# Kernel tuning notes

Measured on AMD Instinct MI355X. Metric: run time of the kernel, lower is better.

Reference implementation:

```python
import jax, jax.numpy as jnp
import numpy as np

NUM_EMBEDDINGS = 1024
EMBEDDING_DIM = 64
COMMITMENT_COST = 0.25


def setup_inputs() -> dict:
    key = jax.random.key(0)
    k1, k2 = jax.random.split(key)
    inputs = jax.random.normal(k1, (64, 2048, EMBEDDING_DIM), dtype=jnp.float32)
    # nn.Embedding weight init: uniform(-1/K, 1/K)
    lim = 1.0 / NUM_EMBEDDINGS
    weight = jax.random.uniform(k2, (NUM_EMBEDDINGS, EMBEDDING_DIM),
                                dtype=jnp.float32, minval=-lim, maxval=lim)
    return {"inputs": inputs, "weight": weight}


def reference(inputs, weight):
    # inputs: [B, T, D], weight: [K, D]
    flat = inputs.reshape(-1, EMBEDDING_DIM)              # [N, D]
    distances = (jnp.sum(flat * flat, axis=1, keepdims=True)
                 + jnp.sum(weight * weight, axis=1)
                 - 2.0 * flat @ weight.T)
    encoding_indices = jnp.argmin(distances, axis=1)[:, None]  # [N, 1]
    quantized = weight[encoding_indices[:, 0]].reshape(inputs.shape)
    # detached quantized vs inputs (commitment), quantized vs detached inputs (codebook)
    e_latent_loss = jnp.mean((jax.lax.stop_gradient(quantized) - inputs) ** 2)
    q_latent_loss = jnp.mean((quantized - jax.lax.stop_gradient(inputs)) ** 2)
    loss = q_latent_loss + COMMITMENT_COST * e_latent_loss
    # straight-through estimator
    quantized_st = inputs + jax.lax.stop_gradient(quantized - inputs)
    return (loss, quantized_st, encoding_indices)
```

## Files before the change

kernel.cpp:

```cpp
#include <hip/hip_runtime.h>

#define NROWS   131072
#define DIM     64
#define K       1024
#define QOFF    1
#define IDXOFF  8388609
#define NSCR    1024
#define NFIN    512

typedef float    f32x4 __attribute__((ext_vector_type(4)));
typedef _Float16 f16x8 __attribute__((ext_vector_type(8)));

__device__ __forceinline__ float np_norm64(const float* v) {
    #pragma clang fp contract(off)
    float r[8];
    #pragma unroll
    for (int k = 0; k < 8; ++k) r[k] = v[k] * v[k];
    #pragma unroll
    for (int i = 8; i < 64; i += 8)
        #pragma unroll
        for (int k = 0; k < 8; ++k) r[k] += v[i + k] * v[i + k];
    return ((r[0] + r[1]) + (r[2] + r[3])) + ((r[4] + r[5]) + (r[6] + r[7]));
}
__device__ __forceinline__ float exact_dot64(const float* xr, const float* __restrict__ e) {
    float a0 = 0.f, a1 = 0.f, a2 = 0.f, a3 = 0.f;
    #pragma unroll
    for (int i = 0; i < 64; i += 4) {
        a0 = fmaf(xr[i + 0], e[i + 0], a0);
        a1 = fmaf(xr[i + 1], e[i + 1], a1);
        a2 = fmaf(xr[i + 2], e[i + 2], a2);
        a3 = fmaf(xr[i + 3], e[i + 3], a3);
    }
    return (a0 + a1) + (a2 + a3);
}
__device__ __forceinline__ float exact_d(float cr, float sej, float dot) {
    #pragma clang fp contract(off)
    float t = cr + sej;
    return t - 2.0f * dot;
}

__global__ void vq_prep(const float* __restrict__ w, unsigned short* __restrict__ Gf,
                        float* __restrict__ wT, float* __restrict__ se,
                        float* __restrict__ se20, int* __restrict__ gcnt) {
    int gid = blockIdx.x * 256 + threadIdx.x;
    if (gid < 2) gcnt[gid] = 0;
    int lane = gid & 63, c = (gid >> 6) & 1, ntile = gid >> 7;
    int code = ntile * 16 + (lane & 15);
    int k0 = c * 32 + (lane >> 4) * 8;
    const float* rowp = w + code * 64 + k0;
    f16x8 h8;
    #pragma unroll
    for (int j = 0; j < 8; ++j) h8[j] = (_Float16)(rowp[j] * 1024.0f);
    *(f16x8*)(Gf + gid * 8) = h8;
    #pragma unroll
    for (int t = 0; t < 8; ++t) {
        int flat = t * 8192 + gid;
        int i = flat >> 10, j = flat & 1023;
        wT[flat] = w[j * 64 + i];
    }
    if (gid < K) {
        #pragma clang fp contract(off)
        const float* e = w + gid * 64;
        float r[8];
        #pragma unroll
        for (int k2 = 0; k2 < 8; ++k2) r[k2] = e[k2] * e[k2];
        #pragma unroll
        for (int i = 8; i < 64; i += 8)
            #pragma unroll
            for (int k2 = 0; k2 < 8; ++k2) r[k2] += e[i + k2] * e[i + k2];
        float v = ((r[0] + r[1]) + (r[2] + r[3])) + ((r[4] + r[5]) + (r[6] + r[7]));
        se[gid] = v;
        se20[gid] = v * 1048576.0f;
    }
}

__global__ __launch_bounds__(256, 4) void vq_screen(
    const float* __restrict__ x, const float* __restrict__ w,
    const unsigned short* __restrict__ Gf, const float* __restrict__ se20,
    float* __restrict__ out, float* __restrict__ partial, int* __restrict__ gcnt,
    int* __restrict__ pairRows, int* __restrict__ pairJJ, int* __restrict__ fullRows) {
    __shared__ float sSe[1024];
    __shared__ float sPart[4];
    __shared__ int sCnt[2], sBase[2];
    __shared__ int sPairRow[128], sPairJJ[128], sFullRow[128];
    const int tid  = threadIdx.x;
    const int wave = tid >> 6, lane = tid & 63;
    const int quad = lane >> 4, m16 = lane & 15;
    const int wrow0 = blockIdx.x * 128 + wave * 32;

    if (tid < 2) sCnt[tid] = 0;
    #pragma unroll
    for (int t = 0; t < 4; ++t) sSe[t * 256 + tid] = se20[t * 256 + tid];

    f16x8 Ah[2][2];
    float Sloc[2] = {0.f, 0.f};
    #pragma unroll
    for (int mt = 0; mt < 2; ++mt)
        #pragma unroll
        for (int c = 0; c < 2; ++c) {
            const float* p = x + (wrow0 + mt * 16 + m16) * 64 + c * 32 + quad * 8;
            f32x4 u0 = *(const f32x4*)p;
            f32x4 u1 = *(const f32x4*)(p + 4);
            #pragma unroll
            for (int j = 0; j < 8; ++j) {
                float xv = (j < 4) ? u0[j] : u1[j - 4];
                Ah[mt][c][j] = (_Float16)xv;
                Sloc[mt] += fabsf(xv);
            }
        }
    #pragma unroll
    for (int mt = 0; mt < 2; ++mt) {
        Sloc[mt] += __shfl_xor(Sloc[mt], 16, 64);
        Sloc[mt] += __shfl_xor(Sloc[mt], 32, 64);
    }

    int m1[2][4], m2[2][4], m3[2][4];
    #pragma unroll
    for (int mt = 0; mt < 2; ++mt)
        #pragma unroll
        for (int r = 0; r < 4; ++r) {
            m1[mt][r] = 0x7fffffff; m2[mt][r] = 0x7fffffff; m3[mt][r] = 0x7fffffff;
        }

    __syncthreads();

    #pragma unroll 8
    for (int t = 0; t < 64; ++t) {
        f16x8 B0 = *(const f16x8*)(Gf + t * 1024 + lane * 8);
        f16x8 B1 = *(const f16x8*)(Gf + t * 1024 + 512 + lane * 8);
        float sen = sSe[t * 16 + m16];
        int jn = t * 16 + m16;
        #pragma unroll
        for (int mt = 0; mt < 2; ++mt) {
            f32x4 acc = {0.f, 0.f, 0.f, 0.f};
            acc = __builtin_amdgcn_mfma_f32_16x16x32_f16(Ah[mt][0], B0, acc, 0, 0, 0);
            acc = __builtin_amdgcn_mfma_f32_16x16x32_f16(Ah[mt][1], B1, acc, 0, 0, 0);
            #pragma unroll
            for (int r = 0; r < 4; ++r) {
                float kf = fmaf(acc[r], -2048.0f, sen);
                int q = (int)kf;
                int key = (int)((unsigned)q << 10) | jn;
                int a  = max(m2[mt][r], key);
                int t2 = max(m1[mt][r], key);
                m3[mt][r] = min(m3[mt][r], a);
                m2[mt][r] = min(m2[mt][r], t2);
                m1[mt][r] = min(m1[mt][r], key);
            }
        }
    }

    #pragma unroll
    for (int mask = 1; mask <= 8; mask <<= 1) {
        #pragma unroll
        for (int mt = 0; mt < 2; ++mt)
            #pragma unroll
            for (int r = 0; r < 4; ++r) {
                int b1 = __shfl_xor(m1[mt][r], mask, 64);
                int b2 = __shfl_xor(m2[mt][r], mask, 64);
                int b3 = __shfl_xor(m3[mt][r], mask, 64);
                int lo1 = min(m1[mt][r], b1), hi1 = max(m1[mt][r], b1);
                int lo2 = min(m2[mt][r], b2);
                m1[mt][r] = lo1;
                m2[mt][r] = min(hi1, lo2);
                m3[mt][r] = min(max(hi1, lo2), min(m3[mt][r], b3));
            }
    }

    int jd[2][4];
    #pragma unroll
    for (int mt = 0; mt < 2; ++mt)
        #pragma unroll
        for (int r = 0; r < 4; ++r) {
            int k1 = m1[mt][r], k2 = m2[mt][r], k3 = m3[mt][r];
            int g21 = (k2 >> 10) - (k1 >> 10);
            int g31 = (k3 >> 10) - (k1 >> 10);
            int j1 = k1 & 1023;
            float Srow = __shfl(Sloc[mt], quad * 4 + r, 64);
            int mq = (int)(Srow * 2.002f) + 5;
            jd[mt][r] = (g21 > mq) ? j1 : -1;
            if (m16 == 0) {
                int rowG = wrow0 + mt * 16 + quad * 4 + r;
                if (g21 > mq) {
                    out[IDXOFF + rowG] = (float)j1;
                } else if (g31 > mq) {
                    int p = atomicAdd(&sCnt[0], 1);
                    sPairRow[p] = rowG; sPairJJ[p] = j1 | ((k2 & 1023) << 10);
                } else {
                    int p = atomicAdd(&sCnt[1], 1);
                    sFullRow[p] = rowG;
                }
            }
        }

    float part = 0.f;
    #pragma unroll
    for (int i = 0; i < 32; ++i) {
        int jr = __shfl(jd[i >> 4][i & 3], ((i & 15) >> 2) * 16, 64);
        if (jr >= 0) {
            #pragma clang fp contract(off)
            int rowG = wrow0 + i;
            float xv = x[rowG * 64 + lane];
            float wv = w[jr * 64 + lane];
            float diff = wv - xv;
            part += diff * diff;
            out[QOFF + rowG * 64 + lane] = xv + diff;
        }
    }
    for (int off = 32; off > 0; off >>= 1) part += __shfl_down(part, off, 64);
    if (lane == 0) sPart[wave] = part;
    __syncthreads();
    if (tid == 0) {
        partial[blockIdx.x] = (sPart[0] + sPart[1]) + (sPart[2] + sPart[3]);
        int np_ = sCnt[0], nf = sCnt[1];
        sBase[0] = np_ ? atomicAdd(&gcnt[0], np_) : 0;
        sBase[1] = nf  ? atomicAdd(&gcnt[1], nf)  : 0;
    }
    __syncthreads();
    if (tid < sCnt[0]) {
        int d = sBase[0] + tid;
        pairRows[d] = sPairRow[tid]; pairJJ[d] = sPairJJ[tid];
    }
    if (tid < sCnt[1]) fullRows[sBase[1] + tid] = sFullRow[tid];
}

__global__ __launch_bounds__(256) void vq_finish(
    const float* __restrict__ x, const float* __restrict__ w, const float* __restrict__ wT,
    const float* __restrict__ se, float* __restrict__ out, float* __restrict__ partial,
    const int* __restrict__ gcnt, const int* __restrict__ pairRows,
    const int* __restrict__ pairJJ, const int* __restrict__ fullRows) {
    __shared__ float sPart[4];
    const int tid = threadIdx.x;
    const int lane = tid & 63, wave = tid >> 6;
    const int nPair = gcnt[0], nFull = gcnt[1];
    const int gthread = blockIdx.x * 256 + tid, nThreads = gridDim.x * 256;
    const int gwave = blockIdx.x * 4 + wave,   nWaves = gridDim.x * 4;
    float part = 0.f;

    for (int i = gthread; i < nPair; i += nThreads) {
        int row = pairRows[i], jj = pairJJ[i];
        int ja = jj & 1023, jb = (jj >> 10) & 1023;
        if (ja > jb) { int t = ja; ja = jb; jb = t; }
        float xr[64];
        const f32x4* xp = (const f32x4*)(x + row * 64);
        #pragma unroll
        for (int t = 0; t < 16; ++t) {
            f32x4 v = xp[t];
            xr[4 * t] = v[0]; xr[4 * t + 1] = v[1]; xr[4 * t + 2] = v[2]; xr[4 * t + 3] = v[3];
        }
        float cr = np_norm64(xr);
        float da = exact_d(cr, se[ja], exact_dot64(xr, w + ja * 64));
        float db = exact_d(cr, se[jb], exact_dot64(xr, w + jb * 64));
        int win = (db < da) ? jb : ja;
        out[IDXOFF + row] = (float)win;
        const float* e = w + win * 64;
        {
            #pragma clang fp contract(off)
            #pragma unroll
            for (int i2 = 0; i2 < 64; ++i2) {
                float diff = e[i2] - xr[i2];
                part += diff * diff;
                out[QOFF + row * 64 + i2] = xr[i2] + diff;
            }
        }
    }

    const f32x4* wT4 = (const f32x4*)wT;
    for (int i = gwave; i < nFull; i += nWaves) {
        int row = fullRows[i];
        float xr[64];
        const f32x4* xp = (const f32x4*)(x + row * 64);
        #pragma unroll
        for (int t = 0; t < 16; ++t) {
            f32x4 v = xp[t];
            xr[4 * t] = v[0]; xr[4 * t + 1] = v[1]; xr[4 * t + 2] = v[2]; xr[4 * t + 3] = v[3];
        }
        float cr = np_norm64(xr);
        float bd = 3.402823466e38f; int bj = 0;
        #pragma unroll
        for (int g = 0; g < 4; ++g) {
            f32x4 a0 = {0.f,0.f,0.f,0.f}, a1 = a0, a2 = a0, a3 = a0;
            #pragma unroll 4
            for (int i2 = 0; i2 < 64; i2 += 4) {
                f32x4 w0 = wT4[(i2 + 0) * 256 + g * 64 + lane];
                f32x4 w1 = wT4[(i2 + 1) * 256 + g * 64 + lane];
                f32x4 w2 = wT4[(i2 + 2) * 256 + g * 64 + lane];
                f32x4 w3 = wT4[(i2 + 3) * 256 + g * 64 + lane];
                #pragma unroll
                for (int c = 0; c < 4; ++c) {
                    a0[c] = fmaf(xr[i2 + 0], w0[c], a0[c]);
                    a1[c] = fmaf(xr[i2 + 1], w1[c], a1[c]);
                    a2[c] = fmaf(xr[i2 + 2], w2[c], a2[c]);
                    a3[c] = fmaf(xr[i2 + 3], w3[c], a3[c]);
                }
            }
            #pragma unroll
            for (int c = 0; c < 4; ++c) {
                float dot = (a0[c] + a1[c]) + (a2[c] + a3[c]);
                int j = g * 256 + lane * 4 + c;
                float d = exact_d(cr, se[j], dot);
                if (d < bd) { bd = d; bj = j; }
            }
        }
        for (int mask = 1; mask < 64; mask <<= 1) {
            float od = __shfl_xor(bd, mask, 64);
            int   oj = __shfl_xor(bj, mask, 64);
            if (od < bd || (od == bd && oj < bj)) { bd = od; bj = oj; }
        }
        {
            #pragma clang fp contract(off)
            float xv = x[row * 64 + lane];
            float wv = w[bj * 64 + lane];
            float diff = wv - xv;
            part += diff * diff;
            out[QOFF + row * 64 + lane] = xv + diff;
        }
        if (lane == 0) out[IDXOFF + row] = (float)bj;
    }

    for (int off = 32; off > 0; off >>= 1) part += __shfl_down(part, off, 64);
    if (lane == 0) sPart[wave] = part;
    __syncthreads();
    if (tid == 0) partial[NSCR + blockIdx.x] = (sPart[0] + sPart[1]) + (sPart[2] + sPart[3]);
}

__global__ __launch_bounds__(256) void vq_loss(const float* __restrict__ partial,
                                               float* __restrict__ out) {
    __shared__ float red[4];
    const int tid = threadIdx.x, lane = tid & 63, wave = tid >> 6;
    float s = 0.f;
    #pragma unroll
    for (int t = 0; t < 6; ++t) s += partial[t * 256 + tid];
    for (int off = 32; off > 0; off >>= 1) s += __shfl_down(s, off, 64);
    if (lane == 0) red[wave] = s;
    __syncthreads();
    if (tid == 0) out[0] = ((red[0] + red[1]) + (red[2] + red[3])) * (1.25f / 8388608.0f);
}

extern "C" void kernel_launch(void* const* d_in, const int* in_sizes, int n_in,
                              void* d_out, int out_size, void* d_ws, size_t ws_size,
                              hipStream_t stream) {
    const float* x = (const float*)d_in[0];
    const float* w = (const float*)d_in[1];
    float* out = (float*)d_out;

    unsigned short* Gf = (unsigned short*)d_ws;
    float* se   = (float*)((char*)d_ws + 131072);
    float* se20 = (float*)((char*)d_ws + 135168);
    float* wT   = (float*)((char*)d_ws + 139264);
    int* gcnt   = (int*)((char*)d_ws + 401408);
    int* pairRows = (int*)((char*)d_ws + 401920);
    int* pairJJ   = pairRows + NROWS;
    int* fullRows = pairJJ + NROWS;
    float* partial = (float*)(fullRows + NROWS);

    vq_prep<<<32, 256, 0, stream>>>(w, Gf, wT, se, se20, gcnt);
    vq_screen<<<NSCR, 256, 0, stream>>>(x, w, Gf, se20, out, partial, gcnt,
                                        pairRows, pairJJ, fullRows);
    vq_finish<<<NFIN, 256, 0, stream>>>(x, w, wT, se, out, partial, gcnt,
                                        pairRows, pairJJ, fullRows);
    vq_loss<<<1, 256, 0, stream>>>(partial, out);
}
```

Measured before the change: 184.7 us.

## Split codebook scan across wave pairs and prefetch B fragments

Each block now covers 64 rows instead of 128, and two waves share each 32-row group, with each wave scanning half of the codebook tiles. The per-wave top-3 candidates are merged through shared memory. The codebook fragments are software-prefetched one tile ahead, and the occupancy hint is raised from 4 to 6 blocks. This doubles the grid and shortens each wave's serial MFMA/min chain to expose more parallelism and hide load latency, at the cost of a shared-memory merge, an extra barrier and idle half-waves during finalisation.

```diff
diff --git a/kernel.cpp b/kernel.cpp
--- a/kernel.cpp
+++ b/kernel.cpp
@@ -5,7 +5,7 @@
 #define K       1024
 #define QOFF    1
 #define IDXOFF  8388609
-#define NSCR    1024
+#define NSCR    2048
 #define NFIN    512
 
 typedef float    f32x4 __attribute__((ext_vector_type(4)));
@@ -74,19 +74,21 @@
     }
 }
 
-__global__ __launch_bounds__(256, 4) void vq_screen(
+__global__ __launch_bounds__(256, 6) void vq_screen(
     const float* __restrict__ x, const float* __restrict__ w,
     const unsigned short* __restrict__ Gf, const float* __restrict__ se20,
     float* __restrict__ out, float* __restrict__ partial, int* __restrict__ gcnt,
     int* __restrict__ pairRows, int* __restrict__ pairJJ, int* __restrict__ fullRows) {
     __shared__ float sSe[1024];
-    __shared__ float sPart[4];
+    __shared__ int   sM[2][32][3];
+    __shared__ float sPart[2];
     __shared__ int sCnt[2], sBase[2];
-    __shared__ int sPairRow[128], sPairJJ[128], sFullRow[128];
+    __shared__ int sPairRow[64], sPairJJ[64], sFullRow[64];
     const int tid  = threadIdx.x;
     const int wave = tid >> 6, lane = tid & 63;
+    const int rg   = wave >> 1, kh = wave & 1;
     const int quad = lane >> 4, m16 = lane & 15;
-    const int wrow0 = blockIdx.x * 128 + wave * 32;
+    const int wrow0 = blockIdx.x * 64 + rg * 32;
 
     if (tid < 2) sCnt[tid] = 0;
     #pragma unroll
@@ -124,17 +126,22 @@
 
     __syncthreads();
 
+    const int t0 = kh * 32;
+    f16x8 B0c = *(const f16x8*)(Gf + t0 * 1024 + lane * 8);
+    f16x8 B1c = *(const f16x8*)(Gf + t0 * 1024 + 512 + lane * 8);
     #pragma unroll 8
-    for (int t = 0; t < 64; ++t) {
-        f16x8 B0 = *(const f16x8*)(Gf + t * 1024 + lane * 8);
-        f16x8 B1 = *(const f16x8*)(Gf + t * 1024 + 512 + lane * 8);
+    for (int tt = 0; tt < 32; ++tt) {
+        int t  = t0 + tt;
+        int tn = (tt < 31) ? t + 1 : t;
+        f16x8 B0n = *(const f16x8*)(Gf + tn * 1024 + lane * 8);
+        f16x8 B1n = *(const f16x8*)(Gf + tn * 1024 + 512 + lane * 8);
         float sen = sSe[t * 16 + m16];
         int jn = t * 16 + m16;
         #pragma unroll
         for (int mt = 0; mt < 2; ++mt) {
             f32x4 acc = {0.f, 0.f, 0.f, 0.f};
-            acc = __builtin_amdgcn_mfma_f32_16x16x32_f16(Ah[mt][0], B0, acc, 0, 0, 0);
-            acc = __builtin_amdgcn_mfma_f32_16x16x32_f16(Ah[mt][1], B1, acc, 0, 0, 0);
+            acc = __builtin_amdgcn_mfma_f32_16x16x32_f16(Ah[mt][0], B0c, acc, 0, 0, 0);
+            acc = __builtin_amdgcn_mfma_f32_16x16x32_f16(Ah[mt][1], B1c, acc, 0, 0, 0);
             #pragma unroll
             for (int r = 0; r < 4; ++r) {
                 float kf = fmaf(acc[r], -2048.0f, sen);
@@ -147,6 +154,7 @@
                 m1[mt][r] = min(m1[mt][r], key);
             }
         }
+        B0c = B0n; B1c = B1n;
     }
 
     #pragma unroll
@@ -166,51 +174,79 @@
             }
     }
 
-    int jd[2][4];
-    #pragma unroll
-    for (int mt = 0; mt < 2; ++mt)
-        #pragma unroll
-        for (int r = 0; r < 4; ++r) {
-            int k1 = m1[mt][r], k2 = m2[mt][r], k3 = m3[mt][r];
-            int g21 = (k2 >> 10) - (k1 >> 10);
-            int g31 = (k3 >> 10) - (k1 >> 10);
-            int j1 = k1 & 1023;
-            float Srow = __shfl(Sloc[mt], quad * 4 + r, 64);
-            int mq = (int)(Srow * 2.002f) + 5;
-            jd[mt][r] = (g21 > mq) ? j1 : -1;
-            if (m16 == 0) {
-                int rowG = wrow0 + mt * 16 + quad * 4 + r;
-                if (g21 > mq) {
-                    out[IDXOFF + rowG] = (float)j1;
-                } else if (g31 > mq) {
-                    int p = atomicAdd(&sCnt[0], 1);
-                    sPairRow[p] = rowG; sPairJJ[p] = j1 | ((k2 & 1023) << 10);
-                } else {
-                    int p = atomicAdd(&sCnt[1], 1);
-                    sFullRow[p] = rowG;
+    if (kh == 1 && m16 == 0) {
+        #pragma unroll
+        for (int mt = 0; mt < 2; ++mt)
+            #pragma unroll
+            for (int r = 0; r < 4; ++r) {
+                int row = mt * 16 + quad * 4 + r;
+                sM[rg][row][0] = m1[mt][r];
+                sM[rg][row][1] = m2[mt][r];
+                sM[rg][row][2] = m3[mt][r];
+            }
+    }
+    __syncthreads();
+
+    if (kh == 0) {
+        #pragma unroll
+        for (int mt = 0; mt < 2; ++mt)
+            #pragma unroll
+            for (int r = 0; r < 4; ++r) {
+                int row = mt * 16 + quad * 4 + r;
+                int b1 = sM[rg][row][0], b2 = sM[rg][row][1], b3 = sM[rg][row][2];
+                int lo1 = min(m1[mt][r], b1), hi1 = max(m1[mt][r], b1);
+                int lo2 = min(m2[mt][r], b2);
+                m1[mt][r] = lo1;
+                m2[mt][r] = min(hi1, lo2);
+                m3[mt][r] = min(max(hi1, lo2), min(m3[mt][r], b3));
+            }
+
+        int jd[2][4];
+        #pragma unroll
+        for (int mt = 0; mt < 2; ++mt)
+            #pragma unroll
+            for (int r = 0; r < 4; ++r) {
+                int k1 = m1[mt][r], k2 = m2[mt][r], k3 = m3[mt][r];
+                int g21 = (k2 >> 10) - (k1 >> 10);
+                int g31 = (k3 >> 10) - (k1 >> 10);
+                int j1 = k1 & 1023;
+                float Srow = __shfl(Sloc[mt], quad * 4 + r, 64);
+                int mq = (int)(Srow * 2.002f) + 5;
+                jd[mt][r] = (g21 > mq) ? j1 : -1;
+                if (m16 == 0) {
+                    int rowG = wrow0 + mt * 16 + quad * 4 + r;
+                    if (g21 > mq) {
+                        out[IDXOFF + rowG] = (float)j1;
+                    } else if (g31 > mq) {
+                        int p = atomicAdd(&sCnt[0], 1);
+                        sPairRow[p] = rowG; sPairJJ[p] = j1 | ((k2 & 1023) << 10);
+                    } else {
+                        int p = atomicAdd(&sCnt[1], 1);
+                        sFullRow[p] = rowG;
+                    }
                 }
             }
-        }
-
-    float part = 0.f;
-    #pragma unroll
-    for (int i = 0; i < 32; ++i) {
-        int jr = __shfl(jd[i >> 4][i & 3], ((i & 15) >> 2) * 16, 64);
-        if (jr >= 0) {
-            #pragma clang fp contract(off)
-            int rowG = wrow0 + i;
-            float xv = x[rowG * 64 + lane];
-            float wv = w[jr * 64 + lane];
-            float diff = wv - xv;
-            part += diff * diff;
-            out[QOFF + rowG * 64 + lane] = xv + diff;
-        }
-    }
-    for (int off = 32; off > 0; off >>= 1) part += __shfl_down(part, off, 64);
-    if (lane == 0) sPart[wave] = part;
+
+        float part = 0.f;
+        #pragma unroll
+        for (int i = 0; i < 32; ++i) {
+            int jr = __shfl(jd[i >> 4][i & 3], ((i & 15) >> 2) * 16, 64);
+            if (jr >= 0) {
+                #pragma clang fp contract(off)
+                int rowG = wrow0 + i;
+                float xv = x[rowG * 64 + lane];
+                float wv = w[jr * 64 + lane];
+                float diff = wv - xv;
+                part += diff * diff;
+                out[QOFF + rowG * 64 + lane] = xv + diff;
+            }
+        }
+        for (int off = 32; off > 0; off >>= 1) part += __shfl_down(part, off, 64);
+        if (lane == 0) sPart[rg] = part;
+    }
     __syncthreads();
     if (tid == 0) {
-        partial[blockIdx.x] = (sPart[0] + sPart[1]) + (sPart[2] + sPart[3]);
+        partial[blockIdx.x] = sPart[0] + sPart[1];
         int np_ = sCnt[0], nf = sCnt[1];
         sBase[0] = np_ ? atomicAdd(&gcnt[0], np_) : 0;
         sBase[1] = nf  ? atomicAdd(&gcnt[1], nf)  : 0;
@@ -329,7 +365,7 @@
     const int tid = threadIdx.x, lane = tid & 63, wave = tid >> 6;
     float s = 0.f;
     #pragma unroll
-    for (int t = 0; t < 6; ++t) s += partial[t * 256 + tid];
+    for (int t = 0; t < 10; ++t) s += partial[t * 256 + tid];
     for (int off = 32; off > 0; off >>= 1) s += __shfl_down(s, off, 64);
     if (lane == 0) red[wave] = s;
     __syncthreads();
```

Result: slower. 194.3 us (+5.2%).

## Fuse finish pass into screen kernel using block-local shared-memory work lists

Applied to the files above, without the earlier changes.

The separate finish kernel and its global work queues (atomic counters, pair/full row arrays) are removed. Each screen block now resolves its own ambiguous rows, both the pair tie-breaks and the full exact-distance rescans, straight from its shared-memory lists after a barrier. This drops a kernel launch, the global atomics and the round trip of the lists through memory. In exchange, load balance gets worse: blocks with many full-rescan rows become stragglers, the screen kernel's register pressure may rise, and pair rows now read x straight from global memory instead of a register copy.

```diff
diff --git a/kernel.cpp b/kernel.cpp
--- a/kernel.cpp
+++ b/kernel.cpp
@@ -6,7 +6,6 @@
 #define QOFF    1
 #define IDXOFF  8388609
 #define NSCR    1024
-#define NFIN    512
 
 typedef float    f32x4 __attribute__((ext_vector_type(4)));
 typedef _Float16 f16x8 __attribute__((ext_vector_type(8)));
@@ -22,7 +21,8 @@
         for (int k = 0; k < 8; ++k) r[k] += v[i + k] * v[i + k];
     return ((r[0] + r[1]) + (r[2] + r[3])) + ((r[4] + r[5]) + (r[6] + r[7]));
 }
-__device__ __forceinline__ float exact_dot64(const float* xr, const float* __restrict__ e) {
+__device__ __forceinline__ float exact_dot64(const float* __restrict__ xr,
+                                             const float* __restrict__ e) {
     float a0 = 0.f, a1 = 0.f, a2 = 0.f, a3 = 0.f;
     #pragma unroll
     for (int i = 0; i < 64; i += 4) {
@@ -41,9 +41,8 @@
 
 __global__ void vq_prep(const float* __restrict__ w, unsigned short* __restrict__ Gf,
                         float* __restrict__ wT, float* __restrict__ se,
-                        float* __restrict__ se20, int* __restrict__ gcnt) {
+                        float* __restrict__ se20) {
     int gid = blockIdx.x * 256 + threadIdx.x;
-    if (gid < 2) gcnt[gid] = 0;
     int lane = gid & 63, c = (gid >> 6) & 1, ntile = gid >> 7;
     int code = ntile * 16 + (lane & 15);
     int k0 = c * 32 + (lane >> 4) * 8;
@@ -77,11 +76,11 @@
 __global__ __launch_bounds__(256, 4) void vq_screen(
     const float* __restrict__ x, const float* __restrict__ w,
     const unsigned short* __restrict__ Gf, const float* __restrict__ se20,
-    float* __restrict__ out, float* __restrict__ partial, int* __restrict__ gcnt,
-    int* __restrict__ pairRows, int* __restrict__ pairJJ, int* __restrict__ fullRows) {
+    const float* __restrict__ se, const float* __restrict__ wT,
+    float* __restrict__ out, float* __restrict__ partial) {
     __shared__ float sSe[1024];
     __shared__ float sPart[4];
-    __shared__ int sCnt[2], sBase[2];
+    __shared__ int sCnt[2];
     __shared__ int sPairRow[128], sPairJJ[128], sFullRow[128];
     const int tid  = threadIdx.x;
     const int wave = tid >> 6, lane = tid & 63;
@@ -206,47 +205,14 @@
             out[QOFF + rowG * 64 + lane] = xv + diff;
         }
     }
-    for (int off = 32; off > 0; off >>= 1) part += __shfl_down(part, off, 64);
-    if (lane == 0) sPart[wave] = part;
     __syncthreads();
-    if (tid == 0) {
-        partial[blockIdx.x] = (sPart[0] + sPart[1]) + (sPart[2] + sPart[3]);
-        int np_ = sCnt[0], nf = sCnt[1];
-        sBase[0] = np_ ? atomicAdd(&gcnt[0], np_) : 0;
-        sBase[1] = nf  ? atomicAdd(&gcnt[1], nf)  : 0;
-    }
-    __syncthreads();
-    if (tid < sCnt[0]) {
-        int d = sBase[0] + tid;
-        pairRows[d] = sPairRow[tid]; pairJJ[d] = sPairJJ[tid];
-    }
-    if (tid < sCnt[1]) fullRows[sBase[1] + tid] = sFullRow[tid];
-}
-
-__global__ __launch_bounds__(256) void vq_finish(
-    const float* __restrict__ x, const float* __restrict__ w, const float* __restrict__ wT,
-    const float* __restrict__ se, float* __restrict__ out, float* __restrict__ partial,
-    const int* __restrict__ gcnt, const int* __restrict__ pairRows,
-    const int* __restrict__ pairJJ, const int* __restrict__ fullRows) {
-    __shared__ float sPart[4];
-    const int tid = threadIdx.x;
-    const int lane = tid & 63, wave = tid >> 6;
-    const int nPair = gcnt[0], nFull = gcnt[1];
-    const int gthread = blockIdx.x * 256 + tid, nThreads = gridDim.x * 256;
-    const int gwave = blockIdx.x * 4 + wave,   nWaves = gridDim.x * 4;
-    float part = 0.f;
-
-    for (int i = gthread; i < nPair; i += nThreads) {
-        int row = pairRows[i], jj = pairJJ[i];
+    const int nP = sCnt[0], nF = sCnt[1];
+
+    for (int p = tid; p < nP; p += 256) {
+        int row = sPairRow[p], jj = sPairJJ[p];
         int ja = jj & 1023, jb = (jj >> 10) & 1023;
         if (ja > jb) { int t = ja; ja = jb; jb = t; }
-        float xr[64];
-        const f32x4* xp = (const f32x4*)(x + row * 64);
-        #pragma unroll
-        for (int t = 0; t < 16; ++t) {
-            f32x4 v = xp[t];
-            xr[4 * t] = v[0]; xr[4 * t + 1] = v[1]; xr[4 * t + 2] = v[2]; xr[4 * t + 3] = v[3];
-        }
+        const float* xr = x + row * 64;
         float cr = np_norm64(xr);
         float da = exact_d(cr, se[ja], exact_dot64(xr, w + ja * 64));
         float db = exact_d(cr, se[jb], exact_dot64(xr, w + jb * 64));
@@ -265,8 +231,8 @@
     }
 
     const f32x4* wT4 = (const f32x4*)wT;
-    for (int i = gwave; i < nFull; i += nWaves) {
-        int row = fullRows[i];
+    for (int f = wave; f < nF; f += 4) {
+        int row = sFullRow[f];
         float xr[64];
         const f32x4* xp = (const f32x4*)(x + row * 64);
         #pragma unroll
@@ -320,7 +286,7 @@
     for (int off = 32; off > 0; off >>= 1) part += __shfl_down(part, off, 64);
     if (lane == 0) sPart[wave] = part;
     __syncthreads();
-    if (tid == 0) partial[NSCR + blockIdx.x] = (sPart[0] + sPart[1]) + (sPart[2] + sPart[3]);
+    if (tid == 0) partial[blockIdx.x] = (sPart[0] + sPart[1]) + (sPart[2] + sPart[3]);
 }
 
 __global__ __launch_bounds__(256) void vq_loss(const float* __restrict__ partial,
@@ -329,7 +295,7 @@
     const int tid = threadIdx.x, lane = tid & 63, wave = tid >> 6;
     float s = 0.f;
     #pragma unroll
-    for (int t = 0; t < 6; ++t) s += partial[t * 256 + tid];
+    for (int t = 0; t < 4; ++t) s += partial[t * 256 + tid];
     for (int off = 32; off > 0; off >>= 1) s += __shfl_down(s, off, 64);
     if (lane == 0) red[wave] = s;
     __syncthreads();
@@ -347,16 +313,9 @@
     float* se   = (float*)((char*)d_ws + 131072);
     float* se20 = (float*)((char*)d_ws + 135168);
     float* wT   = (float*)((char*)d_ws + 139264);
-    int* gcnt   = (int*)((char*)d_ws + 401408);
-    int* pairRows = (int*)((char*)d_ws + 401920);
-    int* pairJJ   = pairRows + NROWS;
-    int* fullRows = pairJJ + NROWS;
-    float* partial = (float*)(fullRows + NROWS);
-
-    vq_prep<<<32, 256, 0, stream>>>(w, Gf, wT, se, se20, gcnt);
-    vq_screen<<<NSCR, 256, 0, stream>>>(x, w, Gf, se20, out, partial, gcnt,
-                                        pairRows, pairJJ, fullRows);
-    vq_finish<<<NFIN, 256, 0, stream>>>(x, w, wT, se, out, partial, gcnt,
-                                        pairRows, pairJJ, fullRows);
+    float* partial = (float*)((char*)d_ws + 401408);
+
+    vq_prep<<<32, 256, 0, stream>>>(w, Gf, wT, se, se20);
+    vq_screen<<<NSCR, 256, 0, stream>>>(x, w, Gf, se20, se, wT, out, partial);
     vq_loss<<<1, 256, 0, stream>>>(partial, out);
 }
```

After: 199.8 us. 1.08x slower.

## Widen prep kernel parallelism and double finish-kernel grid size

Applied to the files above, without the earlier changes.

The prep kernel moves from 32 to 256 blocks. Each thread now does one transpose element, blocks are split into fp16 packing and norm roles, and the codebook norms are computed by 8 lanes per code with xor-shuffle reductions. The finish kernel grid doubles from 512 to 1024 blocks, and the loss reduction reads 2048 partials to match. The aim is to shorten the serial prep stage and spread the finish work over more CUs; it assumes vq_finish handles a larger grid correctly, and the norm summation order changes, which may shift argmin ties.

```diff
diff --git a/kernel.cpp b/kernel.cpp
--- a/kernel.cpp
+++ b/kernel.cpp
@@ -6,7 +6,7 @@
 #define QOFF    1
 #define IDXOFF  8388609
 #define NSCR    1024
-#define NFIN    512
+#define NFIN    1024
 
 typedef float    f32x4 __attribute__((ext_vector_type(4)));
 typedef _Float16 f16x8 __attribute__((ext_vector_type(8)));
@@ -22,7 +22,8 @@
         for (int k = 0; k < 8; ++k) r[k] += v[i + k] * v[i + k];
     return ((r[0] + r[1]) + (r[2] + r[3])) + ((r[4] + r[5]) + (r[6] + r[7]));
 }
-__device__ __forceinline__ float exact_dot64(const float* xr, const float* __restrict__ e) {
+__device__ __forceinline__ float exact_dot64(const float* __restrict__ xr,
+                                             const float* __restrict__ e) {
     float a0 = 0.f, a1 = 0.f, a2 = 0.f, a3 = 0.f;
     #pragma unroll
     for (int i = 0; i < 64; i += 4) {
@@ -39,38 +40,37 @@
     return t - 2.0f * dot;
 }
 
-__global__ void vq_prep(const float* __restrict__ w, unsigned short* __restrict__ Gf,
-                        float* __restrict__ wT, float* __restrict__ se,
-                        float* __restrict__ se20, int* __restrict__ gcnt) {
-    int gid = blockIdx.x * 256 + threadIdx.x;
-    if (gid < 2) gcnt[gid] = 0;
-    int lane = gid & 63, c = (gid >> 6) & 1, ntile = gid >> 7;
-    int code = ntile * 16 + (lane & 15);
-    int k0 = c * 32 + (lane >> 4) * 8;
-    const float* rowp = w + code * 64 + k0;
-    f16x8 h8;
-    #pragma unroll
-    for (int j = 0; j < 8; ++j) h8[j] = (_Float16)(rowp[j] * 1024.0f);
-    *(f16x8*)(Gf + gid * 8) = h8;
-    #pragma unroll
-    for (int t = 0; t < 8; ++t) {
-        int flat = t * 8192 + gid;
-        int i = flat >> 10, j = flat & 1023;
-        wT[flat] = w[j * 64 + i];
-    }
-    if (gid < K) {
+__global__ __launch_bounds__(256) void vq_prep(
+    const float* __restrict__ w, unsigned short* __restrict__ Gf,
+    float* __restrict__ wT, float* __restrict__ se, float* __restrict__ se20,
+    int* __restrict__ gcnt) {
+    const int b = blockIdx.x, t = threadIdx.x;
+    const int g = b * 256 + t;
+    if (g < 2) gcnt[g] = 0;
+    wT[g] = w[(g & 1023) * 64 + (g >> 10)];
+    if (b < 32) {
+        int gid = g;
+        int lane = gid & 63, c = (gid >> 6) & 1, ntile = gid >> 7;
+        int code = ntile * 16 + (lane & 15);
+        int k0 = c * 32 + (lane >> 4) * 8;
+        const float* rowp = w + code * 64 + k0;
+        f16x8 h8;
+        #pragma unroll
+        for (int j = 0; j < 8; ++j) h8[j] = (_Float16)(rowp[j] * 1024.0f);
+        *(f16x8*)(Gf + gid * 8) = h8;
+    } else if (b < 64) {
         #pragma clang fp contract(off)
-        const float* e = w + gid * 64;
-        float r[8];
-        #pragma unroll
-        for (int k2 = 0; k2 < 8; ++k2) r[k2] = e[k2] * e[k2];
-        #pragma unroll
-        for (int i = 8; i < 64; i += 8)
-            #pragma unroll
-            for (int k2 = 0; k2 < 8; ++k2) r[k2] += e[i + k2] * e[i + k2];
-        float v = ((r[0] + r[1]) + (r[2] + r[3])) + ((r[4] + r[5]) + (r[6] + r[7]));
-        se[gid] = v;
-        se20[gid] = v * 1048576.0f;
+        int wv = (b - 32) * 4 + (t >> 6);
+        int k = t & 63;
+        int code = wv * 8 + (k >> 3), st = k & 7;
+        const float* e = w + code * 64 + st;
+        float r = 0.f;
+        #pragma unroll
+        for (int i = 0; i < 8; ++i) { float v = e[8 * i]; r += v * v; }
+        r += __shfl_xor(r, 1, 64);
+        r += __shfl_xor(r, 2, 64);
+        r += __shfl_xor(r, 4, 64);
+        if (st == 0) { se[code] = r; se20[code] = r * 1048576.0f; }
     }
 }
 
@@ -329,7 +329,7 @@
     const int tid = threadIdx.x, lane = tid & 63, wave = tid >> 6;
     float s = 0.f;
     #pragma unroll
-    for (int t = 0; t < 6; ++t) s += partial[t * 256 + tid];
+    for (int t = 0; t < 8; ++t) s += partial[t * 256 + tid];
     for (int off = 32; off > 0; off >>= 1) s += __shfl_down(s, off, 64);
     if (lane == 0) red[wave] = s;
     __syncthreads();
@@ -353,7 +353,7 @@
     int* fullRows = pairJJ + NROWS;
     float* partial = (float*)(fullRows + NROWS);
 
-    vq_prep<<<32, 256, 0, stream>>>(w, Gf, wT, se, se20, gcnt);
+    vq_prep<<<256, 256, 0, stream>>>(w, Gf, wT, se, se20, gcnt);
     vq_screen<<<NSCR, 256, 0, stream>>>(x, w, Gf, se20, out, partial, gcnt,
                                         pairRows, pairJJ, fullRows);
     vq_finish<<<NFIN, 256, 0, stream>>>(x, w, wT, se, out, partial, gcnt,
```

After: 181.6 us. Within noise of the previous version (-1.7%).
